# Performance work log

Hardware: AMD Instinct MI355X
Metric: run time of the kernel (lower is better)

The kernel has to match this reference:

```python
import jax, jax.numpy as jnp
import numpy as np
import math

B, H, S, D = 8, 16, 1024, 64

def setup_inputs() -> dict:
    key = jax.random.key(0)
    kq, kk, kv, km = jax.random.split(key, 4)
    queries = jax.random.normal(kq, (B, H, S, D), dtype=jnp.float32)
    keys = jax.random.normal(kk, (B, H, S, D), dtype=jnp.float32)
    values = jax.random.normal(kv, (B, H, S, D), dtype=jnp.float32)
    mask = jax.random.randint(km, (B, 1, S, S), 0, 2, dtype=jnp.int32)
    return {"queries": queries, "keys": keys, "values": values, "mask": mask}

def reference(queries, keys, values, mask):
    d = values.shape[3]
    # scores: [B,H,S,S] = Q @ K^T / sqrt(d)
    scores = jnp.einsum('bhqd,bhkd->bhqk', queries, keys) / math.sqrt(d)
    attn = jax.nn.softmax(scores, axis=-1)
    # Faithful to source: mask applied AFTER softmax via masked_fill(mask==0, -100000)
    attn = jnp.where(mask == 0, jnp.float32(-100000.0), attn)
    out = jnp.einsum('bhqk,bhkd->bhqd', attn, values)
    return (out, attn)
```

## Files before the change

### kernel.cpp

```cpp
#include <hip/hip_runtime.h>

constexpr int Bm = 8, Hm = 16, Sm = 1024, Dm = 64;
constexpr int BH = Bm * Hm;
constexpr int NBLK = BH * (Sm / 16);

typedef short short8  __attribute__((ext_vector_type(8)));
typedef float floatx4 __attribute__((ext_vector_type(4)));
typedef int   intx4   __attribute__((ext_vector_type(4)));

__device__ inline unsigned short f2bf(float f) {
    unsigned u = __builtin_bit_cast(unsigned, f);
    u += 0x7fffu + ((u >> 16) & 1u);
    return (unsigned short)(u >> 16);
}
__device__ inline float bf2f(unsigned short h) {
    unsigned u = ((unsigned)h) << 16;
    return __builtin_bit_cast(float, u);
}

__global__ __launch_bounds__(256)
void preconv(const float* __restrict__ K, const float* __restrict__ V,
             unsigned short* __restrict__ Kbf, unsigned short* __restrict__ VT)
{
    __shared__ unsigned short tile[64][72];

    const int blk = blockIdx.x;
    const int bh  = blk >> 4;
    const int t   = blk & 15;
    const int tid = threadIdx.x;
    const int row = tid >> 2;
    const int c0  = (tid & 3) << 4;

    {
        const float* src = K + ((size_t)bh * Sm + t * 64 + row) * Dm + c0;
        unsigned short* dst = Kbf + ((size_t)bh * Sm + t * 64 + row) * Dm + c0;
        floatx4 a0 = *(const floatx4*)(src);
        floatx4 a1 = *(const floatx4*)(src + 4);
        floatx4 a2 = *(const floatx4*)(src + 8);
        floatx4 a3 = *(const floatx4*)(src + 12);
        short8 p0, p1;
        #pragma unroll
        for (int i = 0; i < 4; ++i) {
            p0[i]     = (short)f2bf(a0[i]);
            p0[i + 4] = (short)f2bf(a1[i]);
            p1[i]     = (short)f2bf(a2[i]);
            p1[i + 4] = (short)f2bf(a3[i]);
        }
        *(short8*)(dst)     = p0;
        *(short8*)(dst + 8) = p1;
    }
    {
        const float* src = V + ((size_t)bh * Sm + t * 64 + row) * Dm + c0;
        floatx4 a0 = *(const floatx4*)(src);
        floatx4 a1 = *(const floatx4*)(src + 4);
        floatx4 a2 = *(const floatx4*)(src + 8);
        floatx4 a3 = *(const floatx4*)(src + 12);
        short8 p0, p1;
        #pragma unroll
        for (int i = 0; i < 4; ++i) {
            p0[i]     = (short)f2bf(a0[i]);
            p0[i + 4] = (short)f2bf(a1[i]);
            p1[i]     = (short)f2bf(a2[i]);
            p1[i + 4] = (short)f2bf(a3[i]);
        }
        *(short8*)(&tile[row][c0])     = p0;
        *(short8*)(&tile[row][c0 + 8]) = p1;
    }
    __syncthreads();
    {
        const int drow = tid >> 2;
        const int kc0  = (tid & 3) << 4;
        unsigned short* dst = VT + ((size_t)bh * Dm + drow) * Sm + t * 64 + kc0;
        short8 p0, p1;
        #pragma unroll
        for (int j = 0; j < 8; ++j) {
            p0[j] = (short)tile[kc0 + j][drow];
            p1[j] = (short)tile[kc0 + 8 + j][drow];
        }
        *(short8*)(dst)     = p0;
        *(short8*)(dst + 8) = p1;
    }
}

__global__ __launch_bounds__(256, 5)
void attn_fused(const float* __restrict__ Q, const unsigned short* __restrict__ Kbf,
                const unsigned short* __restrict__ VT, const int* __restrict__ Msk,
                float* __restrict__ Gmx,
                float* __restrict__ Out, float* __restrict__ Attn)
{
    __shared__ __align__(16) unsigned short strip[16 * 1024];

    const int tid  = threadIdx.x;
    const int wave = tid >> 6;
    const int lane = tid & 63;
    const int quad = lane >> 4;
    const int ln   = lane & 15;

    const int bid = (blockIdx.x & 7) * (NBLK >> 3) + (blockIdx.x >> 3);
    const int bh = bid >> 6;
    const int qt = bid & 63;
    const int q0 = qt << 4;
    const int b  = bh >> 4;

    const float* Qb = Q + (size_t)bh * (Sm * Dm);
    const unsigned short* Kb = Kbf + (size_t)bh * (Sm * Dm);
    const unsigned short* Vb = VT + (size_t)bh * (Dm * Sm);

    short8 aq0, aq1;
    {
        const float* qrow = Qb + (q0 + ln) * Dm + quad * 8;
        floatx4 a = *(const floatx4*)(qrow);
        floatx4 c = *(const floatx4*)(qrow + 4);
        floatx4 d = *(const floatx4*)(qrow + 32);
        floatx4 e = *(const floatx4*)(qrow + 36);
        #pragma unroll
        for (int i = 0; i < 4; ++i) {
            aq0[i]     = (short)f2bf(a[i] * 0.125f);
            aq0[i + 4] = (short)f2bf(c[i] * 0.125f);
            aq1[i]     = (short)f2bf(d[i] * 0.125f);
            aq1[i + 4] = (short)f2bf(e[i] * 0.125f);
        }
    }

    float rm[4] = {-1e30f, -1e30f, -1e30f, -1e30f};
    for (int kt = wave * 16; kt < wave * 16 + 16; ++kt) {
        const unsigned short* krow = Kb + (kt * 16 + ln) * Dm + quad * 8;
        short8 b0 = *(const short8*)(krow);
        short8 b1 = *(const short8*)(krow + 32);
        floatx4 c = {0.f, 0.f, 0.f, 0.f};
        c = __builtin_amdgcn_mfma_f32_16x16x32_bf16(aq0, b0, c, 0, 0, 0);
        c = __builtin_amdgcn_mfma_f32_16x16x32_bf16(aq1, b1, c, 0, 0, 0);
        const int colb = kt * 16 + ln;
        #pragma unroll
        for (int r = 0; r < 4; ++r) {
            const int row = quad * 4 + r;
            rm[r] = fmaxf(rm[r], c[r]);
            strip[row * 1024 + (colb ^ ((row & 7) << 3))] = f2bf(c[r]);
        }
    }
    #pragma unroll
    for (int off = 8; off >= 1; off >>= 1)
        #pragma unroll
        for (int r = 0; r < 4; ++r)
            rm[r] = fmaxf(rm[r], __shfl_xor(rm[r], off, 16));
    if (ln == 0) {
        float* g = Gmx + ((size_t)bid << 6) + wave * 16 + quad * 4;
        g[0] = rm[0]; g[1] = rm[1]; g[2] = rm[2]; g[3] = rm[3];
    }
    __syncthreads();

    {
        const int row = tid >> 4, l = tid & 15;
        const int sw  = (row & 7) << 3;
        unsigned short* srow = strip + row * 1024;

        const float* g = Gmx + ((size_t)bid << 6) + row;
        float mx = fmaxf(fmaxf(g[0], g[16]), fmaxf(g[32], g[48]));
        mx = bf2f(f2bf(mx));

        float sum = 0.f;
        #pragma unroll
        for (int i = 0; i < 8; ++i) {
            unsigned short* p8 = srow + ((l * 8 + i * 128) ^ sw);
            short8 v = *(const short8*)p8;
            short8 e;
            #pragma unroll
            for (int j = 0; j < 8; ++j) {
                float x = __expf(bf2f((unsigned short)v[j]) - mx);
                sum += x;
                e[j] = (short)f2bf(x);
            }
            *(short8*)p8 = e;
        }
        #pragma unroll
        for (int off = 8; off >= 1; off >>= 1) sum += __shfl_xor(sum, off, 16);
        const float rn = 1.f / sum;

        const int* mrow  = Msk + (size_t)b * (Sm * Sm) + (size_t)(q0 + row) * Sm;
        float*     arow  = Attn + ((size_t)bh * Sm + (q0 + row)) * Sm;
        #pragma unroll
        for (int i = 0; i < 8; ++i) {
            const int c0 = l * 8 + i * 128;
            unsigned short* p8 = srow + (c0 ^ sw);
            short8 v  = *(const short8*)p8;
            intx4  m0 = *(const intx4*)(mrow + c0);
            intx4  m1 = *(const intx4*)(mrow + c0 + 4);
            float p[8];
            #pragma unroll
            for (int j = 0; j < 4; ++j) {
                p[j]     = (m0[j] != 0) ? bf2f((unsigned short)v[j])     * rn : -100000.f;
                p[j + 4] = (m1[j] != 0) ? bf2f((unsigned short)v[j + 4]) * rn : -100000.f;
            }
            floatx4 o0, o1;
            short8 pf;
            #pragma unroll
            for (int j = 0; j < 4; ++j) { o0[j] = p[j]; o1[j] = p[j + 4]; }
            #pragma unroll
            for (int j = 0; j < 8; ++j) pf[j] = (short)f2bf(p[j]);
            *(short8*)p8 = pf;
            *(floatx4*)(arow + c0)     = o0;
            *(floatx4*)(arow + c0 + 4) = o1;
        }
    }
    __syncthreads();

    floatx4 acc[4] = {{0,0,0,0},{0,0,0,0},{0,0,0,0},{0,0,0,0}};
    for (int kb = wave * 256; kb < wave * 256 + 256; kb += 32) {
        short8 af = *(const short8*)(strip + ln * 1024 + ((kb + quad * 8) ^ ((ln & 7) << 3)));
        const unsigned short* vbase = Vb + kb + quad * 8;
        #pragma unroll
        for (int n0 = 0; n0 < 4; ++n0) {
            short8 bf = *(const short8*)(vbase + (size_t)(n0 * 16 + ln) * Sm);
            acc[n0] = __builtin_amdgcn_mfma_f32_16x16x32_bf16(af, bf, acc[n0], 0, 0, 0);
        }
    }
    __syncthreads();

    float* part = (float*)strip;
    #pragma unroll
    for (int n0 = 0; n0 < 4; ++n0)
        #pragma unroll
        for (int r = 0; r < 4; ++r)
            part[wave * 1024 + (quad * 4 + r) * 64 + n0 * 16 + ln] = acc[n0][r];
    __syncthreads();
    {
        const int o4 = tid * 4;
        floatx4 s = *(const floatx4*)(part + o4);
        s += *(const floatx4*)(part + 1024 + o4);
        s += *(const floatx4*)(part + 2048 + o4);
        s += *(const floatx4*)(part + 3072 + o4);
        const int row = o4 >> 6, dc = o4 & 63;
        *(floatx4*)(Out + (size_t)bh * (Sm * Dm) + (size_t)(q0 + row) * Dm + dc) = s;
    }
}

__global__ __launch_bounds__(256, 4)
void attn_fused_f32(const float* __restrict__ Q, const float* __restrict__ K,
                    const float* __restrict__ V, const int* __restrict__ Msk,
                    float* __restrict__ Out, float* __restrict__ Attn)
{
    constexpr int STRIDE = 1040;
    __shared__ __align__(16) unsigned short strip[16 * STRIDE];

    const int tid  = threadIdx.x;
    const int wave = tid >> 6;
    const int lane = tid & 63;
    const int quad = lane >> 4;
    const int ln   = lane & 15;

    const int bid = (blockIdx.x & 7) * (NBLK >> 3) + (blockIdx.x >> 3);
    const int bh = bid >> 6;
    const int qt = bid & 63;
    const int q0 = qt << 4;
    const int b  = bh >> 4;

    const float* Qb = Q + (size_t)bh * (Sm * Dm);
    const float* Kb = K + (size_t)bh * (Sm * Dm);
    const float* Vb = V + (size_t)bh * (Sm * Dm);

    short8 aq0, aq1;
    {
        const float* qrow = Qb + (q0 + ln) * Dm + quad * 8;
        floatx4 a = *(const floatx4*)(qrow);
        floatx4 c = *(const floatx4*)(qrow + 4);
        floatx4 d = *(const floatx4*)(qrow + 32);
        floatx4 e = *(const floatx4*)(qrow + 36);
        #pragma unroll
        for (int i = 0; i < 4; ++i) {
            aq0[i]     = (short)f2bf(a[i] * 0.125f);
            aq0[i + 4] = (short)f2bf(c[i] * 0.125f);
            aq1[i]     = (short)f2bf(d[i] * 0.125f);
            aq1[i + 4] = (short)f2bf(e[i] * 0.125f);
        }
    }

    for (int kt = wave * 16; kt < wave * 16 + 16; ++kt) {
        const float* krow = Kb + (kt * 16 + ln) * Dm + quad * 8;
        floatx4 k0 = *(const floatx4*)(krow);
        floatx4 k1 = *(const floatx4*)(krow + 4);
        floatx4 k2 = *(const floatx4*)(krow + 32);
        floatx4 k3 = *(const floatx4*)(krow + 36);
        short8 b0, b1;
        #pragma unroll
        for (int i = 0; i < 4; ++i) {
            b0[i]     = (short)f2bf(k0[i]);
            b0[i + 4] = (short)f2bf(k1[i]);
            b1[i]     = (short)f2bf(k2[i]);
            b1[i + 4] = (short)f2bf(k3[i]);
        }
        floatx4 c = {0.f, 0.f, 0.f, 0.f};
        c = __builtin_amdgcn_mfma_f32_16x16x32_bf16(aq0, b0, c, 0, 0, 0);
        c = __builtin_amdgcn_mfma_f32_16x16x32_bf16(aq1, b1, c, 0, 0, 0);
        const int colb = kt * 16 + ln;
        #pragma unroll
        for (int r = 0; r < 4; ++r)
            strip[(quad * 4 + r) * STRIDE + colb] = f2bf(c[r]);
    }
    __syncthreads();

    {
        const int row = tid >> 4, l = tid & 15;
        unsigned short* srow = strip + row * STRIDE;

        float mx = -1e30f;
        #pragma unroll
        for (int i = 0; i < 8; ++i) {
            short8 v = *(const short8*)(srow + l * 8 + i * 128);
            #pragma unroll
            for (int j = 0; j < 8; ++j) mx = fmaxf(mx, bf2f((unsigned short)v[j]));
        }
        #pragma unroll
        for (int off = 8; off >= 1; off >>= 1) mx = fmaxf(mx, __shfl_xor(mx, off, 16));

        float sum = 0.f;
        #pragma unroll
        for (int i = 0; i < 8; ++i) {
            short8 v = *(const short8*)(srow + l * 8 + i * 128);
            short8 e;
            #pragma unroll
            for (int j = 0; j < 8; ++j) {
                float x = __expf(bf2f((unsigned short)v[j]) - mx);
                sum += x;
                e[j] = (short)f2bf(x);
            }
            *(short8*)(srow + l * 8 + i * 128) = e;
        }
        #pragma unroll
        for (int off = 8; off >= 1; off >>= 1) sum += __shfl_xor(sum, off, 16);
        const float rn = 1.f / sum;

        const int* mrow  = Msk + (size_t)b * (Sm * Sm) + (size_t)(q0 + row) * Sm;
        float*     arow  = Attn + ((size_t)bh * Sm + (q0 + row)) * Sm;
        #pragma unroll
        for (int i = 0; i < 8; ++i) {
            const int c0 = l * 8 + i * 128;
            short8 v  = *(const short8*)(srow + c0);
            intx4  m0 = *(const intx4*)(mrow + c0);
            intx4  m1 = *(const intx4*)(mrow + c0 + 4);
            float p[8];
            #pragma unroll
            for (int j = 0; j < 4; ++j) {
                p[j]     = (m0[j] != 0) ? bf2f((unsigned short)v[j])     * rn : -100000.f;
                p[j + 4] = (m1[j] != 0) ? bf2f((unsigned short)v[j + 4]) * rn : -100000.f;
            }
            floatx4 o0, o1;
            short8 pf;
            #pragma unroll
            for (int j = 0; j < 4; ++j) { o0[j] = p[j]; o1[j] = p[j + 4]; }
            #pragma unroll
            for (int j = 0; j < 8; ++j) pf[j] = (short)f2bf(p[j]);
            *(short8*)(srow + c0) = pf;
            *(floatx4*)(arow + c0)     = o0;
            *(floatx4*)(arow + c0 + 4) = o1;
        }
    }
    __syncthreads();

    floatx4 acc[4] = {{0,0,0,0},{0,0,0,0},{0,0,0,0},{0,0,0,0}};
    for (int kb = wave * 256; kb < wave * 256 + 256; kb += 32) {
        short8 af = *(const short8*)(strip + ln * STRIDE + kb + quad * 8);
        const float* vbase = Vb + (kb + quad * 8) * Dm + ln;
        #pragma unroll
        for (int n0 = 0; n0 < 4; ++n0) {
            short8 bf;
            #pragma unroll
            for (int j = 0; j < 8; ++j)
                bf[j] = (short)f2bf(vbase[j * Dm + n0 * 16]);
            acc[n0] = __builtin_amdgcn_mfma_f32_16x16x32_bf16(af, bf, acc[n0], 0, 0, 0);
        }
    }
    __syncthreads();

    float* part = (float*)strip;
    #pragma unroll
    for (int n0 = 0; n0 < 4; ++n0)
        #pragma unroll
        for (int r = 0; r < 4; ++r)
            part[wave * 1024 + (quad * 4 + r) * 64 + n0 * 16 + ln] = acc[n0][r];
    __syncthreads();
    {
        const int o4 = tid * 4;
        floatx4 s = *(const floatx4*)(part + o4);
        s += *(const floatx4*)(part + 1024 + o4);
        s += *(const floatx4*)(part + 2048 + o4);
        s += *(const floatx4*)(part + 3072 + o4);
        const int row = o4 >> 6, dc = o4 & 63;
        *(floatx4*)(Out + (size_t)bh * (Sm * Dm) + (size_t)(q0 + row) * Dm + dc) = s;
    }
}

extern "C" void kernel_launch(void* const* d_in, const int* in_sizes, int n_in,
                              void* d_out, int out_size, void* d_ws, size_t ws_size,
                              hipStream_t stream)
{
    const float* Q   = (const float*)d_in[0];
    const float* K   = (const float*)d_in[1];
    const float* V   = (const float*)d_in[2];
    const int*   Msk = (const int*)d_in[3];
    float* Out  = (float*)d_out;
    float* Attn = Out + (size_t)Bm * Hm * Sm * Dm;

    const size_t nElem = (size_t)BH * Sm * Dm;
    const size_t bfBytes = nElem * 2 * sizeof(unsigned short);
    const size_t gmxBytes = (size_t)NBLK * 64 * sizeof(float);
    const size_t need = bfBytes + gmxBytes;

    if (d_ws != nullptr && ws_size >= need) {
        unsigned short* Kbf = (unsigned short*)d_ws;
        unsigned short* VT  = Kbf + nElem;
        float*          Gmx = (float*)(VT + nElem);
        preconv<<<dim3(BH * 16), dim3(256), 0, stream>>>(K, V, Kbf, VT);
        attn_fused<<<dim3(NBLK), dim3(256), 0, stream>>>(Q, Kbf, VT, Msk, Gmx, Out, Attn);
    } else {
        attn_fused_f32<<<dim3(NBLK), dim3(256), 0, stream>>>(Q, K, V, Msk, Out, Attn);
    }
}
```

Measured before the change: 882.8 us.

## Pack mask into bitmask, keep row max in shared memory

Adds a maskpack kernel that turns the int32 mask into a bitmask with wave ballots, so the attention kernel reads one byte per 8 columns instead of 32 bytes. The mask is shared across all 16 heads, so attn_fused repeatedly re-reads it, and the packed form shrinks that traffic by 32x. The per-wave row maxima now go through a small shared array instead of a global workspace. The occupancy hint drops from 5 to 4 blocks per CU, and the extra kernel launch plus one full pass over the mask adds some cost.

Measured after the change: 866.7 us. No clear change (-1.8%).

```diff
diff --git a/kernel.cpp b/kernel.cpp
--- a/kernel.cpp
+++ b/kernel.cpp
@@ -82,13 +82,29 @@
     }
 }
 
-__global__ __launch_bounds__(256, 5)
+__global__ __launch_bounds__(256)
+void maskpack(const int* __restrict__ Msk, unsigned long long* __restrict__ Mb)
+{
+    const int row  = blockIdx.x;
+    const int wave = threadIdx.x >> 6;
+    const int lane = threadIdx.x & 63;
+    const int* src = Msk + (size_t)row * Sm;
+    #pragma unroll
+    for (int p = 0; p < 4; ++p) {
+        const int col = wave * 256 + p * 64 + lane;
+        unsigned long long m = __ballot(src[col] != 0);
+        if (lane == 0) Mb[(size_t)row * 16 + wave * 4 + p] = m;
+    }
+}
+
+__global__ __launch_bounds__(256, 4)
 void attn_fused(const float* __restrict__ Q, const unsigned short* __restrict__ Kbf,
-                const unsigned short* __restrict__ VT, const int* __restrict__ Msk,
-                float* __restrict__ Gmx,
+                const unsigned short* __restrict__ VT,
+                const unsigned long long* __restrict__ Mb,
                 float* __restrict__ Out, float* __restrict__ Attn)
 {
     __shared__ __align__(16) unsigned short strip[16 * 1024];
+    __shared__ float smax[4][16];
 
     const int tid  = threadIdx.x;
     const int wave = tid >> 6;
@@ -144,8 +160,8 @@
         for (int r = 0; r < 4; ++r)
             rm[r] = fmaxf(rm[r], __shfl_xor(rm[r], off, 16));
     if (ln == 0) {
-        float* g = Gmx + ((size_t)bid << 6) + wave * 16 + quad * 4;
-        g[0] = rm[0]; g[1] = rm[1]; g[2] = rm[2]; g[3] = rm[3];
+        #pragma unroll
+        for (int r = 0; r < 4; ++r) smax[wave][quad * 4 + r] = rm[r];
     }
     __syncthreads();
 
@@ -154,8 +170,8 @@
         const int sw  = (row & 7) << 3;
         unsigned short* srow = strip + row * 1024;
 
-        const float* g = Gmx + ((size_t)bid << 6) + row;
-        float mx = fmaxf(fmaxf(g[0], g[16]), fmaxf(g[32], g[48]));
+        float mx = fmaxf(fmaxf(smax[0][row], smax[1][row]),
+                         fmaxf(smax[2][row], smax[3][row]));
         mx = bf2f(f2bf(mx));
 
         float sum = 0.f;
@@ -176,21 +192,19 @@
         for (int off = 8; off >= 1; off >>= 1) sum += __shfl_xor(sum, off, 16);
         const float rn = 1.f / sum;
 
-        const int* mrow  = Msk + (size_t)b * (Sm * Sm) + (size_t)(q0 + row) * Sm;
-        float*     arow  = Attn + ((size_t)bh * Sm + (q0 + row)) * Sm;
+        const unsigned char* mrow =
+            (const unsigned char*)(Mb + ((size_t)b * Sm + (q0 + row)) * 16);
+        float* arow = Attn + ((size_t)bh * Sm + (q0 + row)) * Sm;
         #pragma unroll
         for (int i = 0; i < 8; ++i) {
             const int c0 = l * 8 + i * 128;
             unsigned short* p8 = srow + (c0 ^ sw);
             short8 v  = *(const short8*)p8;
-            intx4  m0 = *(const intx4*)(mrow + c0);
-            intx4  m1 = *(const intx4*)(mrow + c0 + 4);
+            const unsigned mu = mrow[l + 16 * i];
             float p[8];
             #pragma unroll
-            for (int j = 0; j < 4; ++j) {
-                p[j]     = (m0[j] != 0) ? bf2f((unsigned short)v[j])     * rn : -100000.f;
-                p[j + 4] = (m1[j] != 0) ? bf2f((unsigned short)v[j + 4]) * rn : -100000.f;
-            }
+            for (int j = 0; j < 8; ++j)
+                p[j] = ((mu >> j) & 1u) ? bf2f((unsigned short)v[j]) * rn : -100000.f;
             floatx4 o0, o1;
             short8 pf;
             #pragma unroll
@@ -402,15 +416,16 @@
 
     const size_t nElem = (size_t)BH * Sm * Dm;
     const size_t bfBytes = nElem * 2 * sizeof(unsigned short);
-    const size_t gmxBytes = (size_t)NBLK * 64 * sizeof(float);
-    const size_t need = bfBytes + gmxBytes;
+    const size_t mbBytes = (size_t)Bm * Sm * 16 * sizeof(unsigned long long);
+    const size_t need = bfBytes + mbBytes;
 
     if (d_ws != nullptr && ws_size >= need) {
         unsigned short* Kbf = (unsigned short*)d_ws;
         unsigned short* VT  = Kbf + nElem;
-        float*          Gmx = (float*)(VT + nElem);
+        unsigned long long* Mb = (unsigned long long*)(VT + nElem);
         preconv<<<dim3(BH * 16), dim3(256), 0, stream>>>(K, V, Kbf, VT);
-        attn_fused<<<dim3(NBLK), dim3(256), 0, stream>>>(Q, Kbf, VT, Msk, Gmx, Out, Attn);
+        maskpack<<<dim3(Bm * Sm), dim3(256), 0, stream>>>(Msk, Mb);
+        attn_fused<<<dim3(NBLK), dim3(256), 0, stream>>>(Q, Kbf, VT, Mb, Out, Attn);
     } else {
         attn_fused_f32<<<dim3(NBLK), dim3(256), 0, stream>>>(Q, K, V, Msk, Out, Attn);
     }
```
